# Performance work log

Measured on AMD Instinct MI355X. Metric: run time of the kernel, lower is better.

The kernel has to match this reference:

```python
import jax, jax.numpy as jnp
import numpy as np

C = 512
NH = 4
HD = C // NH
G = 32  # min(32, C) and C % 32 == 0
EPS = 1e-5


def setup_inputs() -> dict:
    key = jax.random.key(0)
    ks = jax.random.split(key, 11)
    s = 1.0 / np.sqrt(C)
    return {
        "x": jax.random.normal(ks[0], (16, C, 32, 32), dtype=jnp.float32),
        "gamma": jnp.ones((C,), jnp.float32),
        "beta": jnp.zeros((C,), jnp.float32),
        "wq": jax.random.normal(ks[1], (C, C), jnp.float32) * s,
        "bq": jax.random.normal(ks[2], (C,), jnp.float32) * 0.01,
        "wk": jax.random.normal(ks[3], (C, C), jnp.float32) * s,
        "bk": jax.random.normal(ks[4], (C,), jnp.float32) * 0.01,
        "wv": jax.random.normal(ks[5], (C, C), jnp.float32) * s,
        "bv": jax.random.normal(ks[6], (C,), jnp.float32) * 0.01,
        "wp": jax.random.normal(ks[7], (C, C), jnp.float32) * s,
        "bp": jax.random.normal(ks[8], (C,), jnp.float32) * 0.01,
    }


def _group_norm(x, gamma, beta):
    b, c, h, w = x.shape
    xr = x.reshape(b, G, c // G, h, w)
    mean = xr.mean(axis=(2, 3, 4), keepdims=True)
    var = xr.var(axis=(2, 3, 4), keepdims=True)
    xn = ((xr - mean) * jax.lax.rsqrt(var + EPS)).reshape(b, c, h, w)
    return xn * gamma[None, :, None, None] + beta[None, :, None, None]


def _conv1x1(x, w, b):
    # 1x1 conv == per-position channel GEMM
    return jnp.einsum('oc,bchw->bohw', w, x) + b[None, :, None, None]


def reference(x, gamma, beta, wq, bq, wk, bk, wv, bv, wp, bp):
    b, c, h, w = x.shape
    hw = h * w
    scale = HD ** (-0.5)
    hn = _group_norm(x, gamma, beta)
    q = _conv1x1(hn, wq, bq).reshape(b, NH, HD, hw)
    k = _conv1x1(hn, wk, bk).reshape(b, NH, HD, hw)
    v = _conv1x1(hn, wv, bv).reshape(b, NH, HD, hw)
    attn = jnp.einsum('bhdq,bhdk->bhqk', q, k) * scale  # [b, nh, hw, hw]
    attn = jax.nn.softmax(attn, axis=-1)
    out = jnp.einsum('bhqk,bhdk->bhdq', attn, v)  # [b, nh, hd, hw]
    out = out.reshape(b, c, h, w)
    out = _conv1x1(out, wp, bp)
    return x + out
```

## Files before the change

kernel.cpp:

```cpp
#include <hip/hip_runtime.h>
#include <math.h>

#define CCH 512
#define NH 4
#define HD 128
#define HW 1024
#define BATCH 16
#define EPS 1e-5f

typedef __attribute__((ext_vector_type(8))) short bfrag;
typedef __attribute__((ext_vector_type(4))) float f4;
typedef __attribute__((ext_vector_type(16))) float f16v;

static __device__ __forceinline__ unsigned short f2bf(float f) {
  union { float f; unsigned u; } v;
  v.f = f;
  unsigned r = v.u + 0x7fff + ((v.u >> 16) & 1);
  return (unsigned short)(r >> 16);
}
static __device__ __forceinline__ unsigned pack2(unsigned short a, unsigned short b) {
  return (unsigned)a | ((unsigned)b << 16);
}
static __device__ __forceinline__ unsigned cvt_pk_bf16(float a, float b) {
  unsigned r;
  asm("v_cvt_pk_bf16_f32 %0, %1, %2" : "=v"(r) : "v"(a), "v"(b));
  return r;
}
#if defined(__has_builtin) && __has_builtin(__builtin_amdgcn_exp2f)
#define EXP2(x) __builtin_amdgcn_exp2f(x)
#else
#define EXP2(x) __expf((x) * 0.6931471805599453f)
#endif
static __device__ __forceinline__ void ldg_lds16(const unsigned short* g,
                                                 unsigned short* l) {
  __builtin_amdgcn_global_load_lds(
      (const __attribute__((address_space(1))) unsigned int*)g,
      (__attribute__((address_space(3))) unsigned int*)l, 16, 0, 0);
}

#define QSCALE (0.08838834764831845f * 1.4426950408889634f)

__global__ __launch_bounds__(256) void wcvt_kernel(const float* __restrict__ s0,
                                                   const float* __restrict__ s1,
                                                   const float* __restrict__ s2,
                                                   const float* __restrict__ s3,
                                                   unsigned short* __restrict__ d) {
  const float* srcs[4] = {s0, s1, s2, s3};
  const float* s = srcs[blockIdx.y];
  unsigned short* dp = d + (size_t)blockIdx.y * CCH * CCH;
  int i = blockIdx.x * 256 + threadIdx.x;
  f4 v = ((const f4*)s)[i];
  ushort4 o;
  o.x = f2bf(v.x); o.y = f2bf(v.y); o.z = f2bf(v.z); o.w = f2bf(v.w);
  ((ushort4*)dp)[i] = o;
}

__global__ __launch_bounds__(256) void gn_kernel(const float* __restrict__ x,
                                                 const float* __restrict__ gamma,
                                                 const float* __restrict__ beta,
                                                 unsigned short* __restrict__ hn) {
  int b = blockIdx.x >> 5, g = blockIdx.x & 31;
  const float* xp = x + ((size_t)b * CCH + g * 16) * HW;
  int t = threadIdx.x;
  float s = 0.f, ss = 0.f;
  const f4* xp4 = (const f4*)xp;
  for (int i = t; i < 4096; i += 256) {
    f4 v = xp4[i];
    s += v.x + v.y + v.z + v.w;
    ss += v.x * v.x + v.y * v.y + v.z * v.z + v.w * v.w;
  }
#pragma unroll
  for (int off = 32; off > 0; off >>= 1) {
    s += __shfl_xor(s, off);
    ss += __shfl_xor(ss, off);
  }
  __shared__ float rs[4], rss[4];
  int w = t >> 6;
  if ((t & 63) == 0) { rs[w] = s; rss[w] = ss; }
  __syncthreads();
  s = rs[0] + rs[1] + rs[2] + rs[3];
  ss = rss[0] + rss[1] + rss[2] + rss[3];
  const float invn = 1.f / (16 * HW);
  float mean = s * invn;
  float var = ss * invn - mean * mean;
  float rstd = rsqrtf(var + EPS);
  float a_[16], b_[16];
#pragma unroll
  for (int c = 0; c < 16; ++c) {
    float gm = gamma[g * 16 + c] * rstd;
    a_[c] = gm;
    b_[c] = beta[g * 16 + c] - mean * gm;
  }
#pragma unroll
  for (int i = 0; i < 4; ++i) {
    int p = t + 256 * i;
    unsigned short tv[16];
#pragma unroll
    for (int c = 0; c < 16; ++c) tv[c] = f2bf(xp[c * HW + p] * a_[c] + b_[c]);
    uint4 u0, u1;
    u0.x = pack2(tv[0], tv[1]);  u0.y = pack2(tv[2], tv[3]);
    u0.z = pack2(tv[4], tv[5]);  u0.w = pack2(tv[6], tv[7]);
    u1.x = pack2(tv[8], tv[9]);  u1.y = pack2(tv[10], tv[11]);
    u1.z = pack2(tv[12], tv[13]); u1.w = pack2(tv[14], tv[15]);
    unsigned short* dst = hn + ((size_t)b * HW + p) * CCH + g * 16;
    *(uint4*)dst = u0;
    *(uint4*)(dst + 8) = u1;
  }
}

template <int PROJ>
__global__ __launch_bounds__(256, 3) void mm_kernel(
    const unsigned short* __restrict__ Xt, const unsigned short* __restrict__ Wb,
    const float* __restrict__ b0, const float* __restrict__ b1,
    const float* __restrict__ b2, const float* __restrict__ resid,
    unsigned short* __restrict__ O0, unsigned short* __restrict__ O1,
    unsigned short* __restrict__ O2, float* __restrict__ Ofp) {
  int b = blockIdx.z;
  int p0 = blockIdx.x * 128;
  int c0g = blockIdx.y * 128;
  __shared__ __align__(16) unsigned short Xs[128 * 32];
  __shared__ __align__(16) unsigned short Ws[128 * 32];
  int t = threadIdx.x;
  int w = t >> 6, lane = t & 63, l15 = lane & 15, quad = lane >> 4;
  int wp = (w & 1) * 64, wc = (w >> 1) * 64;
  const unsigned short* Xb = Xt + (size_t)b * HW * CCH;
  const unsigned short* Wr = Wb + (size_t)c0g * CCH;
  f4 acc[4][4] = {};
  for (int k0 = 0; k0 < CCH; k0 += 32) {
    __syncthreads();
#pragma unroll
    for (int j = 0; j < 2; ++j) {
      int chk = w * 2 + j;
      int r = chk * 16 + (lane >> 2);
      int c = (lane & 3) ^ (r & 3);
      ldg_lds16(&Xb[(size_t)(p0 + r) * CCH + k0 + c * 8], &Xs[chk * 512]);
      ldg_lds16(&Wr[(size_t)r * CCH + k0 + c * 8], &Ws[chk * 512]);
    }
    __syncthreads();
    bfrag af[4], bf[4];
#pragma unroll
    for (int pt = 0; pt < 4; ++pt) {
      int r = wp + pt * 16 + l15;
      af[pt] = *(const bfrag*)&Xs[r * 32 + (quad ^ (r & 3)) * 8];
    }
#pragma unroll
    for (int ct = 0; ct < 4; ++ct) {
      int r = wc + ct * 16 + l15;
      bf[ct] = *(const bfrag*)&Ws[r * 32 + (quad ^ (r & 3)) * 8];
    }
#pragma unroll
    for (int pt = 0; pt < 4; ++pt)
#pragma unroll
      for (int ct = 0; ct < 4; ++ct)
        acc[pt][ct] = __builtin_amdgcn_mfma_f32_16x16x32_bf16(
            af[pt], bf[ct], acc[pt][ct], 0, 0, 0);
  }
  if (PROJ) {
#pragma unroll
    for (int ct = 0; ct < 4; ++ct) {
      int ch = c0g + wc + ct * 16 + l15;
      float bi = b0[ch];
#pragma unroll
      for (int pt = 0; pt < 4; ++pt) {
        int pos = p0 + wp + pt * 16 + quad * 4;
        f4 v = acc[pt][ct];
        size_t off = (size_t)b * CCH * HW + (size_t)ch * HW + pos;
        float4 rv = *(const float4*)&resid[off];
        float4 st;
        st.x = v.x + bi + rv.x; st.y = v.y + bi + rv.y;
        st.z = v.z + bi + rv.z; st.w = v.w + bi + rv.w;
        *(float4*)&Ofp[off] = st;
      }
    }
  } else {
    int mat = c0g >> 9;
    int c0 = c0g & 511;
    const float* bias = mat == 0 ? b0 : (mat == 1 ? b1 : b2);
    unsigned short* O = mat == 0 ? O0 : (mat == 1 ? O1 : O2);
    const float sc = (mat == 0) ? QSCALE : 1.0f;
#pragma unroll
    for (int ct = 0; ct < 4; ++ct) {
      int ch = c0 + wc + ct * 16 + l15;
      float bi = bias[ch];
#pragma unroll
      for (int pt = 0; pt < 4; ++pt) {
        int pos = p0 + wp + pt * 16 + quad * 4;
        f4 v = acc[pt][ct];
        if (mat < 2) {
          unsigned short* Op = O + (size_t)b * HW * CCH;
          Op[(size_t)(pos + 0) * CCH + ch] = f2bf((v.x + bi) * sc);
          Op[(size_t)(pos + 1) * CCH + ch] = f2bf((v.y + bi) * sc);
          Op[(size_t)(pos + 2) * CCH + ch] = f2bf((v.z + bi) * sc);
          Op[(size_t)(pos + 3) * CCH + ch] = f2bf((v.w + bi) * sc);
        } else {
          unsigned short* Op = O + (size_t)b * CCH * HW;
          ushort4 st;
          st.x = f2bf(v.x + bi); st.y = f2bf(v.y + bi);
          st.z = f2bf(v.z + bi); st.w = f2bf(v.w + bi);
          *(ushort4*)&Op[(size_t)ch * HW + pos] = st;
        }
      }
    }
  }
}

__global__ __launch_bounds__(256, 2) void attn_kernel(
    const unsigned short* __restrict__ Qt, const unsigned short* __restrict__ Kt,
    const unsigned short* __restrict__ Vc, unsigned short* __restrict__ Ot) {
  int bh = blockIdx.x;
  int b = bh >> 2, h = bh & 3;
  int q0 = blockIdx.y * 128;
  int t = threadIdx.x;
  int w = t >> 6, lane = t & 63;
  int l31 = lane & 31, half = lane >> 5;
  __shared__ __align__(16) unsigned short Ks[2][64 * 128];
  __shared__ __align__(16) unsigned short Vs[2][128 * 64];
  int q = q0 + w * 32 + l31;
  const unsigned short* Kbase = Kt + (size_t)b * HW * CCH + h * HD;
  const unsigned short* Vbase = Vc + ((size_t)b * CCH + h * HD) * HW;
  bfrag qf[8];
#pragma unroll
  for (int ks = 0; ks < 8; ++ks)
    qf[ks] = *(const bfrag*)&Qt[((size_t)b * HW + q) * CCH + h * HD +
                                ks * 16 + half * 8];
  f16v o[4] = {};
  float ls[4] = {};
  auto stage = [&](int kt, int bi) {
    int kk0 = kt * 64;
#pragma unroll
    for (int j = 0; j < 4; ++j) {
      int chk = w * 4 + j;
      {
        int r = chk * 4 + (lane >> 4);
        int c = (lane & 15) ^ (r & 15);
        ldg_lds16(&Kbase[(size_t)(kk0 + r) * CCH + c * 8], &Ks[bi][chk * 512]);
      }
      {
        int r = chk * 8 + (lane >> 3);
        int c = (lane & 7) ^ (r & 7);
        ldg_lds16(&Vbase[(size_t)r * HW + kk0 + c * 8], &Vs[bi][chk * 512]);
      }
    }
  };
  stage(0, 0);
  for (int kt = 0; kt < 16; ++kt) {
    __syncthreads();
    if (kt < 15) stage(kt + 1, (kt + 1) & 1);
    const unsigned short* K_ = Ks[kt & 1];
    const unsigned short* V_ = Vs[kt & 1];
    f16v S[2] = {};
    __builtin_amdgcn_s_setprio(1);
#pragma unroll
    for (int ks = 0; ks < 8; ++ks) {
      int c16 = ks * 2 + half;
#pragma unroll
      for (int mt = 0; mt < 2; ++mt) {
        int r = mt * 32 + l31;
        bfrag kf = *(const bfrag*)&K_[r * 128 + ((c16 ^ (r & 15)) << 3)];
        S[mt] = __builtin_amdgcn_mfma_f32_32x32x16_bf16(kf, qf[ks], S[mt],
                                                        0, 0, 0);
      }
    }
    __builtin_amdgcn_s_setprio(0);
    unsigned pd[16];
#pragma unroll
    for (int mt = 0; mt < 2; ++mt)
#pragma unroll
      for (int i = 0; i < 8; ++i) {
        float p0 = EXP2(S[mt][2 * i]);
        float p1 = EXP2(S[mt][2 * i + 1]);
        ls[i & 3] += p0 + p1;
        pd[mt * 8 + i] = cvt_pk_bf16(p0, p1);
      }
#pragma unroll
    for (int mt = 0; mt < 2; ++mt)
#pragma unroll
      for (int s = 0; s < 2; ++s) {
        int base = mt * 8 + s * 4;
        unsigned s0 = half ? pd[base + 0] : pd[base + 2];
        unsigned s1 = half ? pd[base + 1] : pd[base + 3];
        unsigned r0 = (unsigned)__shfl_xor((int)s0, 32);
        unsigned r1 = (unsigned)__shfl_xor((int)s1, 32);
        union { unsigned u[4]; bfrag f; } pf;
        pf.u[0] = half ? r0 : pd[base + 0];
        pf.u[1] = half ? r1 : pd[base + 1];
        pf.u[2] = half ? pd[base + 2] : r0;
        pf.u[3] = half ? pd[base + 3] : r1;
        int c8 = (mt * 2 + s) * 2 + half;
        __builtin_amdgcn_s_setprio(1);
#pragma unroll
        for (int dt = 0; dt < 4; ++dt) {
          int r = dt * 32 + l31;
          bfrag vf = *(const bfrag*)&V_[r * 64 + ((c8 ^ (r & 7)) << 3)];
          o[dt] = __builtin_amdgcn_mfma_f32_32x32x16_bf16(vf, pf.f, o[dt],
                                                          0, 0, 0);
        }
        __builtin_amdgcn_s_setprio(0);
      }
  }
  float lrow = (ls[0] + ls[1]) + (ls[2] + ls[3]);
  lrow += __shfl_xor(lrow, 32);
  float inv = 1.f / lrow;
  unsigned short* Op = Ot + ((size_t)b * HW + q) * CCH + h * HD;
#pragma unroll
  for (int dt = 0; dt < 4; ++dt)
#pragma unroll
    for (int rg = 0; rg < 4; ++rg) {
      int d = dt * 32 + rg * 8 + half * 4;
      uint2 st;
      st.x = cvt_pk_bf16(o[dt][rg * 4 + 0] * inv, o[dt][rg * 4 + 1] * inv);
      st.y = cvt_pk_bf16(o[dt][rg * 4 + 2] * inv, o[dt][rg * 4 + 3] * inv);
      *(uint2*)&Op[d] = st;
    }
}

extern "C" void kernel_launch(void* const* d_in, const int* in_sizes, int n_in,
                              void* d_out, int out_size, void* d_ws,
                              size_t ws_size, hipStream_t stream) {
  const float* x = (const float*)d_in[0];
  const float* gamma = (const float*)d_in[1];
  const float* beta = (const float*)d_in[2];
  const float* wq = (const float*)d_in[3];
  const float* bq = (const float*)d_in[4];
  const float* wk = (const float*)d_in[5];
  const float* bk = (const float*)d_in[6];
  const float* wv = (const float*)d_in[7];
  const float* bv = (const float*)d_in[8];
  const float* wp = (const float*)d_in[9];
  const float* bp = (const float*)d_in[10];

  const size_t TS = (size_t)BATCH * HW * CCH;
  unsigned short* wB = (unsigned short*)d_ws;
  unsigned short* hn = wB + (size_t)4 * CCH * CCH;
  unsigned short* Qt = hn + TS;
  unsigned short* Kt = Qt + TS;
  unsigned short* Vc = Kt + TS;
  unsigned short* Ot = hn;

  wcvt_kernel<<<dim3(256, 4), 256, 0, stream>>>(wq, wk, wv, wp, wB);
  gn_kernel<<<dim3(BATCH * 32), 256, 0, stream>>>(x, gamma, beta, hn);
  mm_kernel<0><<<dim3(8, 12, BATCH), 256, 0, stream>>>(
      hn, wB, bq, bk, bv, nullptr, Qt, Kt, Vc, nullptr);
  attn_kernel<<<dim3(64, 8), 256, 0, stream>>>(Qt, Kt, Vc, Ot);
  mm_kernel<1><<<dim3(8, 4, BATCH), 256, 0, stream>>>(
      Ot, wB + (size_t)3 * CCH * CCH, bp, bp, bp, x, nullptr, nullptr, nullptr,
      (float*)d_out);
}
```

Baseline: 222.6 us.

## Split attention key tiles across two wave groups and cache GroupNorm inputs in registers

The attention kernel moves to 512-thread blocks. Each query group is handled by two waves that each take half of every 64-key tile, and their partial outputs and row sums are combined through shared memory at the end. The P fragment exchange now uses v_permlane32_swap instead of two shuffles with selects. GroupNorm keeps the 16 loaded float4 values in registers so x is not re-read in the normalize pass, which changes the order in which positions are written. The aim is more waves per CU and fewer global reads, at the cost of extra registers, barriers and an LDS reduction at the end.

```diff
diff --git a/kernel.cpp b/kernel.cpp
--- a/kernel.cpp
+++ b/kernel.cpp
@@ -64,8 +64,11 @@
   int t = threadIdx.x;
   float s = 0.f, ss = 0.f;
   const f4* xp4 = (const f4*)xp;
-  for (int i = t; i < 4096; i += 256) {
-    f4 v = xp4[i];
+  f4 vv[16];
+#pragma unroll
+  for (int c = 0; c < 16; ++c) {
+    f4 v = xp4[c * 256 + t];
+    vv[c] = v;
     s += v.x + v.y + v.z + v.w;
     ss += v.x * v.x + v.y * v.y + v.z * v.z + v.w * v.w;
   }
@@ -93,15 +96,16 @@
   }
 #pragma unroll
   for (int i = 0; i < 4; ++i) {
-    int p = t + 256 * i;
-    unsigned short tv[16];
-#pragma unroll
-    for (int c = 0; c < 16; ++c) tv[c] = f2bf(xp[c * HW + p] * a_[c] + b_[c]);
+    int p = 4 * t + i;
     uint4 u0, u1;
-    u0.x = pack2(tv[0], tv[1]);  u0.y = pack2(tv[2], tv[3]);
-    u0.z = pack2(tv[4], tv[5]);  u0.w = pack2(tv[6], tv[7]);
-    u1.x = pack2(tv[8], tv[9]);  u1.y = pack2(tv[10], tv[11]);
-    u1.z = pack2(tv[12], tv[13]); u1.w = pack2(tv[14], tv[15]);
+    u0.x = cvt_pk_bf16(vv[0][i] * a_[0] + b_[0], vv[1][i] * a_[1] + b_[1]);
+    u0.y = cvt_pk_bf16(vv[2][i] * a_[2] + b_[2], vv[3][i] * a_[3] + b_[3]);
+    u0.z = cvt_pk_bf16(vv[4][i] * a_[4] + b_[4], vv[5][i] * a_[5] + b_[5]);
+    u0.w = cvt_pk_bf16(vv[6][i] * a_[6] + b_[6], vv[7][i] * a_[7] + b_[7]);
+    u1.x = cvt_pk_bf16(vv[8][i] * a_[8] + b_[8], vv[9][i] * a_[9] + b_[9]);
+    u1.y = cvt_pk_bf16(vv[10][i] * a_[10] + b_[10], vv[11][i] * a_[11] + b_[11]);
+    u1.z = cvt_pk_bf16(vv[12][i] * a_[12] + b_[12], vv[13][i] * a_[13] + b_[13]);
+    u1.w = cvt_pk_bf16(vv[14][i] * a_[14] + b_[14], vv[15][i] * a_[15] + b_[15]);
     unsigned short* dst = hn + ((size_t)b * HW + p) * CCH + g * 16;
     *(uint4*)dst = u0;
     *(uint4*)(dst + 8) = u1;
@@ -204,7 +208,7 @@
   }
 }
 
-__global__ __launch_bounds__(256, 2) void attn_kernel(
+__global__ __launch_bounds__(512, 4) void attn_kernel(
     const unsigned short* __restrict__ Qt, const unsigned short* __restrict__ Kt,
     const unsigned short* __restrict__ Vc, unsigned short* __restrict__ Ot) {
   int bh = blockIdx.x;
@@ -213,9 +217,9 @@
   int t = threadIdx.x;
   int w = t >> 6, lane = t & 63;
   int l31 = lane & 31, half = lane >> 5;
-  __shared__ __align__(16) unsigned short Ks[2][64 * 128];
-  __shared__ __align__(16) unsigned short Vs[2][128 * 64];
-  int q = q0 + w * 32 + l31;
+  int qg = w & 3, kh = w >> 2;
+  __shared__ __align__(16) unsigned short S_[32768];
+  int q = q0 + qg * 32 + l31;
   const unsigned short* Kbase = Kt + (size_t)b * HW * CCH + h * HD;
   const unsigned short* Vbase = Vc + ((size_t)b * CCH + h * HD) * HW;
   bfrag qf[8];
@@ -227,18 +231,20 @@
   float ls[4] = {};
   auto stage = [&](int kt, int bi) {
     int kk0 = kt * 64;
-#pragma unroll
-    for (int j = 0; j < 4; ++j) {
-      int chk = w * 4 + j;
+    unsigned short* Kd = S_ + bi * 8192;
+    unsigned short* Vd = S_ + 16384 + bi * 8192;
+#pragma unroll
+    for (int j = 0; j < 2; ++j) {
+      int chk = w * 2 + j;
       {
         int r = chk * 4 + (lane >> 4);
         int c = (lane & 15) ^ (r & 15);
-        ldg_lds16(&Kbase[(size_t)(kk0 + r) * CCH + c * 8], &Ks[bi][chk * 512]);
+        ldg_lds16(&Kbase[(size_t)(kk0 + r) * CCH + c * 8], Kd + chk * 512);
       }
       {
         int r = chk * 8 + (lane >> 3);
         int c = (lane & 7) ^ (r & 7);
-        ldg_lds16(&Vbase[(size_t)r * HW + kk0 + c * 8], &Vs[bi][chk * 512]);
+        ldg_lds16(&Vbase[(size_t)r * HW + kk0 + c * 8], Vd + chk * 512);
       }
     }
   };
@@ -246,72 +252,87 @@
   for (int kt = 0; kt < 16; ++kt) {
     __syncthreads();
     if (kt < 15) stage(kt + 1, (kt + 1) & 1);
-    const unsigned short* K_ = Ks[kt & 1];
-    const unsigned short* V_ = Vs[kt & 1];
-    f16v S[2] = {};
+    const unsigned short* K_ = S_ + (kt & 1) * 8192;
+    const unsigned short* V_ = S_ + 16384 + (kt & 1) * 8192;
+    f16v S = {};
     __builtin_amdgcn_s_setprio(1);
 #pragma unroll
     for (int ks = 0; ks < 8; ++ks) {
       int c16 = ks * 2 + half;
-#pragma unroll
-      for (int mt = 0; mt < 2; ++mt) {
-        int r = mt * 32 + l31;
-        bfrag kf = *(const bfrag*)&K_[r * 128 + ((c16 ^ (r & 15)) << 3)];
-        S[mt] = __builtin_amdgcn_mfma_f32_32x32x16_bf16(kf, qf[ks], S[mt],
+      int r = kh * 32 + l31;
+      bfrag kf = *(const bfrag*)&K_[r * 128 + ((c16 ^ (r & 15)) << 3)];
+      S = __builtin_amdgcn_mfma_f32_32x32x16_bf16(kf, qf[ks], S, 0, 0, 0);
+    }
+    __builtin_amdgcn_s_setprio(0);
+    unsigned pd[8];
+#pragma unroll
+    for (int i = 0; i < 8; ++i) {
+      float p0 = EXP2(S[2 * i]);
+      float p1 = EXP2(S[2 * i + 1]);
+      ls[i & 3] += p0 + p1;
+      pd[i] = cvt_pk_bf16(p0, p1);
+    }
+#pragma unroll
+    for (int s = 0; s < 2; ++s) {
+      unsigned a0 = pd[s * 4 + 0], a1 = pd[s * 4 + 1];
+      unsigned c0 = pd[s * 4 + 2], c1 = pd[s * 4 + 3];
+      asm("v_permlane32_swap_b32 %0, %1" : "+v"(a0), "+v"(c0));
+      asm("v_permlane32_swap_b32 %0, %1" : "+v"(a1), "+v"(c1));
+      union { unsigned u[4]; bfrag f; } pf;
+      pf.u[0] = a0; pf.u[1] = a1; pf.u[2] = c0; pf.u[3] = c1;
+      int c8 = (kh * 2 + s) * 2 + half;
+      __builtin_amdgcn_s_setprio(1);
+#pragma unroll
+      for (int dt = 0; dt < 4; ++dt) {
+        int r = dt * 32 + l31;
+        bfrag vf = *(const bfrag*)&V_[r * 64 + ((c8 ^ (r & 7)) << 3)];
+        o[dt] = __builtin_amdgcn_mfma_f32_32x32x16_bf16(vf, pf.f, o[dt],
                                                         0, 0, 0);
       }
-    }
-    __builtin_amdgcn_s_setprio(0);
-    unsigned pd[16];
-#pragma unroll
-    for (int mt = 0; mt < 2; ++mt)
-#pragma unroll
-      for (int i = 0; i < 8; ++i) {
-        float p0 = EXP2(S[mt][2 * i]);
-        float p1 = EXP2(S[mt][2 * i + 1]);
-        ls[i & 3] += p0 + p1;
-        pd[mt * 8 + i] = cvt_pk_bf16(p0, p1);
-      }
-#pragma unroll
-    for (int mt = 0; mt < 2; ++mt)
-#pragma unroll
-      for (int s = 0; s < 2; ++s) {
-        int base = mt * 8 + s * 4;
-        unsigned s0 = half ? pd[base + 0] : pd[base + 2];
-        unsigned s1 = half ? pd[base + 1] : pd[base + 3];
-        unsigned r0 = (unsigned)__shfl_xor((int)s0, 32);
-        unsigned r1 = (unsigned)__shfl_xor((int)s1, 32);
-        union { unsigned u[4]; bfrag f; } pf;
-        pf.u[0] = half ? r0 : pd[base + 0];
-        pf.u[1] = half ? r1 : pd[base + 1];
-        pf.u[2] = half ? pd[base + 2] : r0;
-        pf.u[3] = half ? pd[base + 3] : r1;
-        int c8 = (mt * 2 + s) * 2 + half;
-        __builtin_amdgcn_s_setprio(1);
-#pragma unroll
-        for (int dt = 0; dt < 4; ++dt) {
-          int r = dt * 32 + l31;
-          bfrag vf = *(const bfrag*)&V_[r * 64 + ((c8 ^ (r & 7)) << 3)];
-          o[dt] = __builtin_amdgcn_mfma_f32_32x32x16_bf16(vf, pf.f, o[dt],
-                                                          0, 0, 0);
-        }
-        __builtin_amdgcn_s_setprio(0);
-      }
+      __builtin_amdgcn_s_setprio(0);
+    }
   }
   float lrow = (ls[0] + ls[1]) + (ls[2] + ls[3]);
   lrow += __shfl_xor(lrow, 32);
-  float inv = 1.f / lrow;
-  unsigned short* Op = Ot + ((size_t)b * HW + q) * CCH + h * HD;
-#pragma unroll
-  for (int dt = 0; dt < 4; ++dt)
-#pragma unroll
-    for (int rg = 0; rg < 4; ++rg) {
-      int d = dt * 32 + rg * 8 + half * 4;
-      uint2 st;
-      st.x = cvt_pk_bf16(o[dt][rg * 4 + 0] * inv, o[dt][rg * 4 + 1] * inv);
-      st.y = cvt_pk_bf16(o[dt][rg * 4 + 2] * inv, o[dt][rg * 4 + 3] * inv);
-      *(uint2*)&Op[d] = st;
-    }
+  __syncthreads();
+  float* lb = (float*)S_;
+  if (kh == 1 && half == 0) lb[qg * 32 + l31] = lrow;
+  __syncthreads();
+  if (kh == 0) lrow += lb[qg * 32 + l31];
+  __syncthreads();
+  float* ob = (float*)S_;
+  if (kh == 1) {
+#pragma unroll
+    for (int dt = 0; dt < 4; ++dt) {
+      union { f16v v; f4 q4[4]; } u; u.v = o[dt];
+#pragma unroll
+      for (int rg = 0; rg < 4; ++rg) {
+        int d4 = dt * 8 + rg * 2 + half;
+        *(f4*)&ob[qg * 4096 + l31 * 128 + ((d4 ^ (l31 & 7)) << 2)] = u.q4[rg];
+      }
+    }
+  }
+  __syncthreads();
+  if (kh == 0) {
+    float inv = 1.f / lrow;
+    unsigned short* Op = Ot + ((size_t)b * HW + q) * CCH + h * HD;
+#pragma unroll
+    for (int dt = 0; dt < 4; ++dt) {
+      union { f16v v; f4 q4[4]; } u; u.v = o[dt];
+#pragma unroll
+      for (int rg = 0; rg < 4; ++rg) {
+        int d4 = dt * 8 + rg * 2 + half;
+        f4 oth = *(const f4*)&ob[qg * 4096 + l31 * 128 +
+                                 ((d4 ^ (l31 & 7)) << 2)];
+        f4 mine = u.q4[rg];
+        int d = d4 << 2;
+        uint2 st;
+        st.x = cvt_pk_bf16((mine.x + oth.x) * inv, (mine.y + oth.y) * inv);
+        st.y = cvt_pk_bf16((mine.z + oth.z) * inv, (mine.w + oth.w) * inv);
+        *(uint2*)&Op[d] = st;
+      }
+    }
+  }
 }
 
 extern "C" void kernel_launch(void* const* d_in, const int* in_sizes, int n_in,
@@ -341,7 +362,7 @@
   gn_kernel<<<dim3(BATCH * 32), 256, 0, stream>>>(x, gamma, beta, hn);
   mm_kernel<0><<<dim3(8, 12, BATCH), 256, 0, stream>>>(
       hn, wB, bq, bk, bv, nullptr, Qt, Kt, Vc, nullptr);
-  attn_kernel<<<dim3(64, 8), 256, 0, stream>>>(Qt, Kt, Vc, Ot);
+  attn_kernel<<<dim3(64, 8), 512, 0, stream>>>(Qt, Kt, Vc, Ot);
   mm_kernel<1><<<dim3(8, 4, BATCH), 256, 0, stream>>>(
       Ot, wB + (size_t)3 * CCH * CCH, bp, bp, bp, x, nullptr, nullptr, nullptr,
       (float*)d_out);
```

Result: slower. 247.5 us (+11.2%).
